# Kernel optimization log

Measured on AMD Instinct MI355X. Metric: run time of the kernel, lower is better.

The kernel has to match this reference:

```python
import jax, jax.numpy as jnp
import numpy as np
import math

B, S, D = 8, 2048, 512
H, DH = 8, 64  # heads, head dim

def setup_inputs() -> dict:
    key = jax.random.key(0)
    ks = jax.random.split(key, 13)
    w = 0.02
    return {
        "x_Q": jax.random.normal(ks[0], (B, S, D), jnp.float32),
        "x_K": jax.random.normal(ks[1], (B, S, D), jnp.float32),
        "x_V": jax.random.normal(ks[2], (B, S, D), jnp.float32),
        "Wq": jax.random.normal(ks[3], (H * DH, D), jnp.float32) * w,
        "bq": jnp.zeros((H * DH,), jnp.float32),
        "Wk": jax.random.normal(ks[4], (H * DH, D), jnp.float32) * w,
        "bk": jnp.zeros((H * DH,), jnp.float32),
        "Wv": jax.random.normal(ks[5], (H * DH, D), jnp.float32) * w,
        "bv": jnp.zeros((H * DH,), jnp.float32),
        "Wo": jax.random.normal(ks[6], (D, H * DH), jnp.float32) * w,
        "bo": jnp.zeros((D,), jnp.float32),
        "src_batch_lens": jax.random.randint(ks[7], (B,), 1, S + 1, jnp.int32),
    }

def reference(x_Q, x_K, x_V, Wq, bq, Wk, bk, Wv, bv, Wo, bo, src_batch_lens):
    b, s, _ = x_Q.shape
    # projections (torch Linear: x @ W.T + b), split into heads
    Q = (x_Q @ Wq.T + bq).reshape(b, s, H, DH)
    K = (x_K @ Wk.T + bk).reshape(b, s, H, DH)
    V = (x_V @ Wv.T + bv).reshape(b, s, H, DH)
    scale = 1.0 / math.sqrt(DH)
    # [b, h, q, k] scores
    scores = jnp.einsum('bqhd,bkhd->bhqk', Q * scale, K)
    # padding mask on key positions >= src_batch_lens[i], filled with -1e9
    key_mask = jnp.arange(s)[None, :] >= src_batch_lens[:, None]  # [b, k]
    scores = jnp.where(key_mask[:, None, None, :], -1.0e9, scores)
    attn = jax.nn.softmax(scores, axis=-1)  # dropout p=0.0 -> identity
    ctx = jnp.einsum('bhqk,bkhd->bqhd', attn, V).reshape(b, s, H * DH)
    return ctx @ Wo.T + bo
```

## Files before the change

### kernel.cpp

```cpp
#include <hip/hip_runtime.h>
#include <math.h>

#define NB 8
#define NS 2048
#define ND 512
#define NHH 8
#define NDH 64

typedef __attribute__((ext_vector_type(4))) float f32x4;
typedef __attribute__((ext_vector_type(8))) short bf16x8;
typedef unsigned short ush;

__device__ inline ush f2bf_rne(float f) {
    unsigned u = __float_as_uint(f);
    unsigned r = u + 0x7FFFu + ((u >> 16) & 1u);
    return (ush)(r >> 16);
}
__device__ inline float bf2f(ush h) { return __uint_as_float(((unsigned)h) << 16); }

__device__ inline unsigned cvt_pk_bf16(float lo, float hi) {
    unsigned r;
    asm("v_cvt_pk_bf16_f32 %0, %1, %2" : "=v"(r) : "v"(lo), "v"(hi));
    return r;
}

#if defined(__has_builtin)
#if __has_builtin(__builtin_amdgcn_exp2f)
#define EXP2F(x) __builtin_amdgcn_exp2f(x)
#else
#define EXP2F(x) exp2f(x)
#endif
#else
#define EXP2F(x) exp2f(x)
#endif

#define GLL16(gp, lp) __builtin_amdgcn_global_load_lds( \
    (const __attribute__((address_space(1))) unsigned int*)(gp), \
    (__attribute__((address_space(3))) unsigned int*)(lp), 16, 0, 0)

__global__ __launch_bounds__(256) void conv_w_kernel(
    const float* __restrict__ Wq, const float* __restrict__ Wk,
    const float* __restrict__ Wv, const float* __restrict__ Wo,
    ush* __restrict__ wbf, ush* __restrict__ wo_hi, ush* __restrict__ wo_lo)
{
    const int y = blockIdx.y;
    const int i = (blockIdx.x * 256 + threadIdx.x) * 4;
    if (y < 3) {
        const float* src = (y == 0) ? Wq : (y == 1) ? Wk : Wv;
        const float4 v = *(const float4*)&src[i];
        ushort4 o;
        o.x = f2bf_rne(v.x); o.y = f2bf_rne(v.y);
        o.z = f2bf_rne(v.z); o.w = f2bf_rne(v.w);
        *(ushort4*)&wbf[y * 262144 + i] = o;
    } else {
        const float4 v = *(const float4*)&Wo[i];
        ushort4 hi, lo;
        hi.x = f2bf_rne(v.x); lo.x = f2bf_rne(v.x - bf2f(hi.x));
        hi.y = f2bf_rne(v.y); lo.y = f2bf_rne(v.y - bf2f(hi.y));
        hi.z = f2bf_rne(v.z); lo.z = f2bf_rne(v.z - bf2f(hi.z));
        hi.w = f2bf_rne(v.w); lo.w = f2bf_rne(v.w - bf2f(hi.w));
        *(ushort4*)&wo_hi[i] = hi;
        *(ushort4*)&wo_lo[i] = lo;
    }
}

__global__ __launch_bounds__(256) void qkv_gemm_kernel(
    const float* __restrict__ xq, const float* __restrict__ xk, const float* __restrict__ xv,
    const ush* __restrict__ wbf,
    const float* __restrict__ bq, const float* __restrict__ bk, const float* __restrict__ bv,
    ush* __restrict__ Qb, ush* __restrict__ Kb, ush* __restrict__ VT)
{
    __shared__ ush As[4096];
    __shared__ ush Bs[4096];

    const int z = blockIdx.z;
    const float* X    = (z == 0) ? xq : (z == 1) ? xk : xv;
    const ush*   W    = wbf + z * 262144;
    const float* bias = (z == 0) ? bq : (z == 1) ? bk : bv;

    const int t = threadIdx.x;
    const int w = t >> 6, l = t & 63;
    const int l15 = l & 15, g = l >> 4;
    const int m0 = blockIdx.x * 128, n0 = blockIdx.y * 128;
    const int wm = (w & 1) << 6, wn = (w >> 1) << 6;

    const int srow = l >> 2;
    const int sg   = (l & 3) ^ ((srow + (srow >> 2)) & 3);
    const int fsw  = (g ^ ((l15 + (l15 >> 2)) & 3)) << 3;
    const int c0   = w * 2;

    f32x4 acc[4][4];
    #pragma unroll
    for (int i = 0; i < 4; ++i)
        #pragma unroll
        for (int j = 0; j < 4; ++j) acc[i][j] = (f32x4)(0.0f);

    for (int kt = 0; kt < 512; kt += 32) {
        const size_t ar0 = (size_t)(m0 + c0 * 16 + srow) * 512 + kt + sg * 8;
        const size_t ar1 = (size_t)(m0 + (c0 + 1) * 16 + srow) * 512 + kt + sg * 8;
        const float4 a0 = *(const float4*)&X[ar0];
        const float4 a1 = *(const float4*)&X[ar0 + 4];
        const float4 a2 = *(const float4*)&X[ar1];
        const float4 a3 = *(const float4*)&X[ar1 + 4];

        __syncthreads();

        GLL16(&W[(size_t)(n0 + c0 * 16 + srow) * 512 + kt + sg * 8], &Bs[c0 * 512 + l * 8]);
        GLL16(&W[(size_t)(n0 + (c0 + 1) * 16 + srow) * 512 + kt + sg * 8], &Bs[(c0 + 1) * 512 + l * 8]);

        uint4 u0, u1;
        u0.x = (unsigned)f2bf_rne(a0.x) | ((unsigned)f2bf_rne(a0.y) << 16);
        u0.y = (unsigned)f2bf_rne(a0.z) | ((unsigned)f2bf_rne(a0.w) << 16);
        u0.z = (unsigned)f2bf_rne(a1.x) | ((unsigned)f2bf_rne(a1.y) << 16);
        u0.w = (unsigned)f2bf_rne(a1.z) | ((unsigned)f2bf_rne(a1.w) << 16);
        u1.x = (unsigned)f2bf_rne(a2.x) | ((unsigned)f2bf_rne(a2.y) << 16);
        u1.y = (unsigned)f2bf_rne(a2.z) | ((unsigned)f2bf_rne(a2.w) << 16);
        u1.z = (unsigned)f2bf_rne(a3.x) | ((unsigned)f2bf_rne(a3.y) << 16);
        u1.w = (unsigned)f2bf_rne(a3.z) | ((unsigned)f2bf_rne(a3.w) << 16);
        *(uint4*)&As[c0 * 512 + l * 8] = u0;
        *(uint4*)&As[(c0 + 1) * 512 + l * 8] = u1;

        __syncthreads();

        bf16x8 af[4], bfr[4];
        #pragma unroll
        for (int mi = 0; mi < 4; ++mi)
            af[mi] = *(const bf16x8*)&As[(((w & 1) << 2) + mi) * 512 + l15 * 32 + fsw];
        #pragma unroll
        for (int ni = 0; ni < 4; ++ni)
            bfr[ni] = *(const bf16x8*)&Bs[(((w >> 1) << 2) + ni) * 512 + l15 * 32 + fsw];
        #pragma unroll
        for (int mi = 0; mi < 4; ++mi)
            #pragma unroll
            for (int ni = 0; ni < 4; ++ni)
                acc[mi][ni] = __builtin_amdgcn_mfma_f32_16x16x32_bf16(af[mi], bfr[ni], acc[mi][ni], 0, 0, 0);
    }

    const float qscale = (z == 0) ? 0.18033688011112042f : 1.0f;
    float bnv[4];
    #pragma unroll
    for (int ni = 0; ni < 4; ++ni) bnv[ni] = bias[n0 + wn + ni * 16 + l15];

    if (z < 2) {
        ush* O = (z == 0) ? Qb : Kb;
        #pragma unroll
        for (int mi = 0; mi < 4; ++mi) {
            #pragma unroll
            for (int ni = 0; ni < 4; ++ni) {
                const int n = n0 + wn + ni * 16 + l15;
                const int hh = n >> 6, dh = n & 63;
                #pragma unroll
                for (int r = 0; r < 4; ++r) {
                    const int m = m0 + wm + mi * 16 + (g << 2) + r;
                    const int bi = m >> 11, s = m & (NS - 1);
                    O[((size_t)(bi * 8 + hh) * 2048 + s) * 64 + dh] =
                        f2bf_rne((acc[mi][ni][r] + bnv[ni]) * qscale);
                }
            }
        }
    } else {
        #pragma unroll
        for (int mi = 0; mi < 4; ++mi) {
            #pragma unroll
            for (int ni = 0; ni < 4; ++ni) {
                const int n = n0 + wn + ni * 16 + l15;
                const int hh = n >> 6, dh = n & 63;
                const int mb = m0 + wm + mi * 16 + (g << 2);
                const int bi = mb >> 11, s = mb & (NS - 1);
                ushort4 pk;
                pk.x = f2bf_rne(acc[mi][ni][0] + bnv[ni]);
                pk.y = f2bf_rne(acc[mi][ni][1] + bnv[ni]);
                pk.z = f2bf_rne(acc[mi][ni][2] + bnv[ni]);
                pk.w = f2bf_rne(acc[mi][ni][3] + bnv[ni]);
                *(ushort4*)&VT[((size_t)(bi * 8 + hh) * 64 + dh) * 2048 + s] = pk;
            }
        }
    }
}

__global__ __launch_bounds__(256) void attn_kernel(
    ush* __restrict__ Qb, const ush* __restrict__ Kb,
    const ush* __restrict__ VT, const int* __restrict__ lens,
    ush* __restrict__ ctx_lo)
{
    __shared__ ush Ps[64 * 72];
    __shared__ ush Vt[4624];

    const int tid = threadIdx.x;
    const int w = tid >> 6, l = tid & 63;
    const int l15 = l & 15, g = l >> 4;

    const int id = blockIdx.x;
    const int h = id & 7, qt = (id >> 3) & 31, b = id >> 8;
    const int L = lens[b];
    const int q0 = qt << 6;
    const size_t bh = ((size_t)b * 8 + h) * 2048;

    const ush* qptr = Qb + (bh + q0 + w * 16 + l15) * 64 + g * 8;
    const bf16x8 qf0 = *(const bf16x8*)(qptr);
    const bf16x8 qf1 = *(const bf16x8*)(qptr + 32);

    const ush* kbase = Kb + (bh + l15) * 64 + g * 8;

    const int dv = tid >> 2, seg = (tid & 3) << 4;
    const ush* vbase = VT + ((size_t)(b * 8 + h) * 64 + dv) * 2048 + seg;
    ush* vt_w = &Vt[dv * 72 + ((dv >> 4) << 3) + seg];

    ush* psw = &Ps[(w * 16 + l15) * 72 + (g << 2)];
    const ush* pp = &Ps[(w * 16 + l15) * 72 + g * 8];

    bf16x8 ones;
    #pragma unroll
    for (int j = 0; j < 8; ++j) ones[j] = (short)0x3F80;

    f32x4 o[4];
    f32x4 ol = (f32x4)(0.0f);
    #pragma unroll
    for (int i = 0; i < 4; ++i) o[i] = (f32x4)(0.0f);

    auto tile = [&](int k0, bool masked) {
        const uint4 v0 = *(const uint4*)(vbase + k0);
        const uint4 v1 = *(const uint4*)(vbase + k0 + 8);

        f32x4 s[4];
        #pragma unroll
        for (int st = 0; st < 4; ++st) s[st] = (f32x4)(0.0f);
        const ush* kp = kbase + (size_t)k0 * 64;
        #pragma unroll
        for (int st = 0; st < 4; ++st) {
            const bf16x8 kf0 = *(const bf16x8*)(kp + st * 16 * 64);
            const bf16x8 kf1 = *(const bf16x8*)(kp + st * 16 * 64 + 32);
            s[st] = __builtin_amdgcn_mfma_f32_16x16x32_bf16(kf0, qf0, s[st], 0, 0, 0);
            s[st] = __builtin_amdgcn_mfma_f32_16x16x32_bf16(kf1, qf1, s[st], 0, 0, 0);
        }

        uint2 pk[4];
        #pragma unroll
        for (int st = 0; st < 4; ++st) {
            float p[4];
            #pragma unroll
            for (int r = 0; r < 4; ++r) {
                float e = EXP2F(s[st][r]);
                if (masked) {
                    const int key = k0 + st * 16 + (g << 2) + r;
                    e = (key < L) ? e : 0.0f;
                }
                p[r] = e;
            }
            pk[st].x = cvt_pk_bf16(p[0], p[1]);
            pk[st].y = cvt_pk_bf16(p[2], p[3]);
        }

        __syncthreads();
        *(uint4*)(vt_w) = v0;
        *(uint4*)(vt_w + 8) = v1;
        #pragma unroll
        for (int st = 0; st < 4; ++st)
            *(uint2*)(psw + st * 16) = pk[st];
        __syncthreads();

        const bf16x8 pf0 = *(const bf16x8*)(pp);
        const bf16x8 pf1 = *(const bf16x8*)(pp + 32);
        ol = __builtin_amdgcn_mfma_f32_16x16x32_bf16(pf0, ones, ol, 0, 0, 0);
        ol = __builtin_amdgcn_mfma_f32_16x16x32_bf16(pf1, ones, ol, 0, 0, 0);
        #pragma unroll
        for (int st2 = 0; st2 < 4; ++st2) {
            const ush* vp = &Vt[(st2 * 16 + l15) * 72 + (st2 << 3) + g * 8];
            const bf16x8 vf0 = *(const bf16x8*)(vp);
            const bf16x8 vf1 = *(const bf16x8*)(vp + 32);
            o[st2] = __builtin_amdgcn_mfma_f32_16x16x32_bf16(pf0, vf0, o[st2], 0, 0, 0);
            o[st2] = __builtin_amdgcn_mfma_f32_16x16x32_bf16(pf1, vf1, o[st2], 0, 0, 0);
        }
    };

    const int nfull = L >> 6;
    for (int kt = 0; kt < nfull; ++kt) tile(kt << 6, false);
    if (L & 63) tile(nfull << 6, true);

    #pragma unroll
    for (int r = 0; r < 4; ++r) {
        const float inv = 1.0f / ol[r];
        const size_t row = bh + q0 + w * 16 + (g << 2) + r;
        #pragma unroll
        for (int st2 = 0; st2 < 4; ++st2) {
            const float val = o[st2][r] * inv;
            const ush hi = f2bf_rne(val);
            const ush lo = f2bf_rne(val - bf2f(hi));
            Qb[row * 64 + st2 * 16 + l15] = hi;
            ctx_lo[row * 64 + st2 * 16 + l15] = lo;
        }
    }
}

__global__ __launch_bounds__(256) void out_gemm_kernel(
    const ush* __restrict__ ctx_hi, const ush* __restrict__ ctx_lo,
    const ush* __restrict__ wo_hi, const ush* __restrict__ wo_lo,
    const float* __restrict__ bo, float* __restrict__ out)
{
    __shared__ ush Ah[4096], Al[4096], Bh[4096], Bl[4096];

    const int t = threadIdx.x;
    const int w = t >> 6, l = t & 63;
    const int l15 = l & 15, g = l >> 4;
    const int m0 = blockIdx.x * 128, n0 = blockIdx.y * 128;
    const int wm = (w & 1) << 6, wn = (w >> 1) << 6;

    const int srow = l >> 2;
    const int sg   = (l & 3) ^ ((srow + (srow >> 2)) & 3);
    const int fsw  = (g ^ ((l15 + (l15 >> 2)) & 3)) << 3;
    const int c0   = w * 2;

    f32x4 acc[4][4];
    #pragma unroll
    for (int i = 0; i < 4; ++i)
        #pragma unroll
        for (int j = 0; j < 4; ++j) acc[i][j] = (f32x4)(0.0f);

    for (int kt = 0; kt < 512; kt += 32) {
        __syncthreads();
        #pragma unroll
        for (int cc = 0; cc < 2; ++cc) {
            const int c = c0 + cc;
            const int m = m0 + c * 16 + srow;
            const int k = kt + sg * 8;
            const size_t ga = ((size_t)((m >> 11) * 8 + (k >> 6)) * 2048 + (m & (NS - 1))) * 64 + (k & 63);
            GLL16(&ctx_hi[ga], &Ah[c * 512 + l * 8]);
            GLL16(&ctx_lo[ga], &Al[c * 512 + l * 8]);
            const size_t gb = (size_t)(n0 + c * 16 + srow) * 512 + kt + sg * 8;
            GLL16(&wo_hi[gb], &Bh[c * 512 + l * 8]);
            GLL16(&wo_lo[gb], &Bl[c * 512 + l * 8]);
        }
        __syncthreads();

        bf16x8 ah[4], al[4], bh4[4], bl4[4];
        #pragma unroll
        for (int mi = 0; mi < 4; ++mi) {
            const int off = (((w & 1) << 2) + mi) * 512 + l15 * 32 + fsw;
            ah[mi] = *(const bf16x8*)&Ah[off];
            al[mi] = *(const bf16x8*)&Al[off];
        }
        #pragma unroll
        for (int ni = 0; ni < 4; ++ni) {
            const int off = (((w >> 1) << 2) + ni) * 512 + l15 * 32 + fsw;
            bh4[ni] = *(const bf16x8*)&Bh[off];
            bl4[ni] = *(const bf16x8*)&Bl[off];
        }
        #pragma unroll
        for (int mi = 0; mi < 4; ++mi)
            #pragma unroll
            for (int ni = 0; ni < 4; ++ni) {
                acc[mi][ni] = __builtin_amdgcn_mfma_f32_16x16x32_bf16(ah[mi], bh4[ni], acc[mi][ni], 0, 0, 0);
                acc[mi][ni] = __builtin_amdgcn_mfma_f32_16x16x32_bf16(al[mi], bh4[ni], acc[mi][ni], 0, 0, 0);
                acc[mi][ni] = __builtin_amdgcn_mfma_f32_16x16x32_bf16(ah[mi], bl4[ni], acc[mi][ni], 0, 0, 0);
            }
    }

    float bov[4];
    #pragma unroll
    for (int ni = 0; ni < 4; ++ni) bov[ni] = bo[n0 + wn + ni * 16 + l15];

    #pragma unroll
    for (int mi = 0; mi < 4; ++mi)
        #pragma unroll
        for (int ni = 0; ni < 4; ++ni) {
            const int n = n0 + wn + ni * 16 + l15;
            #pragma unroll
            for (int r = 0; r < 4; ++r) {
                const int m = m0 + wm + mi * 16 + (g << 2) + r;
                out[(size_t)m * 512 + n] = acc[mi][ni][r] + bov[ni];
            }
        }
}

extern "C" void kernel_launch(void* const* d_in, const int* in_sizes, int n_in,
                              void* d_out, int out_size, void* d_ws, size_t ws_size,
                              hipStream_t stream)
{
    const float* xq   = (const float*)d_in[0];
    const float* xk   = (const float*)d_in[1];
    const float* xv   = (const float*)d_in[2];
    const float* Wq   = (const float*)d_in[3];
    const float* bq   = (const float*)d_in[4];
    const float* Wk   = (const float*)d_in[5];
    const float* bk   = (const float*)d_in[6];
    const float* Wv   = (const float*)d_in[7];
    const float* bv   = (const float*)d_in[8];
    const float* Wo   = (const float*)d_in[9];
    const float* bo   = (const float*)d_in[10];
    const int*   lens = (const int*)d_in[11];
    float* out = (float*)d_out;

    const size_t elems = (size_t)NB * NHH * NS * NDH;
    ush* Qb     = (ush*)d_ws;
    ush* Kb     = Qb + elems;
    ush* VT     = Kb + elems;
    ush* ctx_lo = VT + elems;
    ush* wbf    = ctx_lo + elems;
    ush* wo_hi  = wbf + 3 * 262144;
    ush* wo_lo  = wo_hi + 262144;

    const dim3 blk(256);
    conv_w_kernel<<<dim3(256, 4), blk, 0, stream>>>(Wq, Wk, Wv, Wo, wbf, wo_hi, wo_lo);
    qkv_gemm_kernel<<<dim3(128, 4, 3), blk, 0, stream>>>(
        xq, xk, xv, wbf, bq, bk, bv, Qb, Kb, VT);
    attn_kernel<<<dim3(NB * NHH * (NS / 64)), blk, 0, stream>>>(Qb, Kb, VT, lens, ctx_lo);
    out_gemm_kernel<<<dim3(128, 4), blk, 0, stream>>>(Qb, ctx_lo, wo_hi, wo_lo, bo, out);
}
```

Before: 357.0 us.

## Load V fragments directly from global into registers, drop LDS staging and barriers

The attention kernel no longer stages the transposed V tile through shared memory. Each wave now reads its V MFMA operands straight from global memory into registers, split into two halves issued around the QK MFMAs. This removes both __syncthreads per tile, since each wave only reads back the P rows it wrote itself. It also adds s_setprio around the MFMA blocks, at the cost of more global/L2 traffic (V is fetched redundantly by all 4 waves) and higher register pressure.

```diff
diff --git a/kernel.cpp b/kernel.cpp
--- a/kernel.cpp
+++ b/kernel.cpp
@@ -184,7 +184,6 @@
     ush* __restrict__ ctx_lo)
 {
     __shared__ ush Ps[64 * 72];
-    __shared__ ush Vt[4624];
 
     const int tid = threadIdx.x;
     const int w = tid >> 6, l = tid & 63;
@@ -201,10 +200,7 @@
     const bf16x8 qf1 = *(const bf16x8*)(qptr + 32);
 
     const ush* kbase = Kb + (bh + l15) * 64 + g * 8;
-
-    const int dv = tid >> 2, seg = (tid & 3) << 4;
-    const ush* vbase = VT + ((size_t)(b * 8 + h) * 64 + dv) * 2048 + seg;
-    ush* vt_w = &Vt[dv * 72 + ((dv >> 4) << 3) + seg];
+    const ush* vfbase = VT + bh * 64 + (size_t)l15 * 2048 + g * 8;
 
     ush* psw = &Ps[(w * 16 + l15) * 72 + (g << 2)];
     const ush* pp = &Ps[(w * 16 + l15) * 72 + g * 8];
@@ -219,13 +215,17 @@
     for (int i = 0; i < 4; ++i) o[i] = (f32x4)(0.0f);
 
     auto tile = [&](int k0, bool masked) {
-        const uint4 v0 = *(const uint4*)(vbase + k0);
-        const uint4 v1 = *(const uint4*)(vbase + k0 + 8);
+        const ush* vp = vfbase + k0;
+        bf16x8 vfA[4], vfB[4];
+        #pragma unroll
+        for (int st2 = 0; st2 < 4; ++st2)
+            vfA[st2] = *(const bf16x8*)(vp + st2 * 16 * 2048);
 
         f32x4 s[4];
         #pragma unroll
         for (int st = 0; st < 4; ++st) s[st] = (f32x4)(0.0f);
         const ush* kp = kbase + (size_t)k0 * 64;
+        __builtin_amdgcn_s_setprio(1);
         #pragma unroll
         for (int st = 0; st < 4; ++st) {
             const bf16x8 kf0 = *(const bf16x8*)(kp + st * 16 * 64);
@@ -233,6 +233,11 @@
             s[st] = __builtin_amdgcn_mfma_f32_16x16x32_bf16(kf0, qf0, s[st], 0, 0, 0);
             s[st] = __builtin_amdgcn_mfma_f32_16x16x32_bf16(kf1, qf1, s[st], 0, 0, 0);
         }
+        __builtin_amdgcn_s_setprio(0);
+
+        #pragma unroll
+        for (int st2 = 0; st2 < 4; ++st2)
+            vfB[st2] = *(const bf16x8*)(vp + st2 * 16 * 2048 + 32);
 
         uint2 pk[4];
         #pragma unroll
@@ -251,26 +256,22 @@
             pk[st].y = cvt_pk_bf16(p[2], p[3]);
         }
 
-        __syncthreads();
-        *(uint4*)(vt_w) = v0;
-        *(uint4*)(vt_w + 8) = v1;
         #pragma unroll
         for (int st = 0; st < 4; ++st)
             *(uint2*)(psw + st * 16) = pk[st];
-        __syncthreads();
-
         const bf16x8 pf0 = *(const bf16x8*)(pp);
         const bf16x8 pf1 = *(const bf16x8*)(pp + 32);
+
+        __builtin_amdgcn_s_setprio(1);
         ol = __builtin_amdgcn_mfma_f32_16x16x32_bf16(pf0, ones, ol, 0, 0, 0);
+        #pragma unroll
+        for (int st2 = 0; st2 < 4; ++st2)
+            o[st2] = __builtin_amdgcn_mfma_f32_16x16x32_bf16(pf0, vfA[st2], o[st2], 0, 0, 0);
         ol = __builtin_amdgcn_mfma_f32_16x16x32_bf16(pf1, ones, ol, 0, 0, 0);
         #pragma unroll
-        for (int st2 = 0; st2 < 4; ++st2) {
-            const ush* vp = &Vt[(st2 * 16 + l15) * 72 + (st2 << 3) + g * 8];
-            const bf16x8 vf0 = *(const bf16x8*)(vp);
-            const bf16x8 vf1 = *(const bf16x8*)(vp + 32);
-            o[st2] = __builtin_amdgcn_mfma_f32_16x16x32_bf16(pf0, vf0, o[st2], 0, 0, 0);
-            o[st2] = __builtin_amdgcn_mfma_f32_16x16x32_bf16(pf1, vf1, o[st2], 0, 0, 0);
-        }
+        for (int st2 = 0; st2 < 4; ++st2)
+            o[st2] = __builtin_amdgcn_mfma_f32_16x16x32_bf16(pf1, vfB[st2], o[st2], 0, 0, 0);
+        __builtin_amdgcn_s_setprio(0);
     };
 
     const int nfull = L >> 6;
```

Measured after the change: 443.1 us. 1.24x slower.

## Software-pipeline attention loop with double-buffered V tile and K prefetch

Applied to the files above, without the earlier changes.

Restructures the attention key loop so the next tile's K fragments and V data are loaded, and its QK^T MFMAs issued, while the current tile's softmax and PV MFMAs finish. V is double-buffered in LDS, which cuts the barriers per tile from two to one. It also wraps the MFMA bursts in s_setprio to favour matrix issue. This doubles the V LDS footprint and raises register pressure from the held K fragments, which may lower occupancy.

```diff
diff --git a/kernel.cpp b/kernel.cpp
--- a/kernel.cpp
+++ b/kernel.cpp
@@ -184,7 +184,7 @@
     ush* __restrict__ ctx_lo)
 {
     __shared__ ush Ps[64 * 72];
-    __shared__ ush Vt[4624];
+    __shared__ ush Vt[2 * 4624];
 
     const int tid = threadIdx.x;
     const int w = tid >> 6, l = tid & 63;
@@ -203,8 +203,8 @@
     const ush* kbase = Kb + (bh + l15) * 64 + g * 8;
 
     const int dv = tid >> 2, seg = (tid & 3) << 4;
-    const ush* vbase = VT + ((size_t)(b * 8 + h) * 64 + dv) * 2048 + seg;
-    ush* vt_w = &Vt[dv * 72 + ((dv >> 4) << 3) + seg];
+    const ush* vbase = VT + bh * 64 + (size_t)dv * 2048 + seg;
+    const int vt_off = dv * 72 + ((dv >> 4) << 3) + seg;
 
     ush* psw = &Ps[(w * 16 + l15) * 72 + (g << 2)];
     const ush* pp = &Ps[(w * 16 + l15) * 72 + g * 8];
@@ -218,31 +218,39 @@
     #pragma unroll
     for (int i = 0; i < 4; ++i) o[i] = (f32x4)(0.0f);
 
-    auto tile = [&](int k0, bool masked) {
-        const uint4 v0 = *(const uint4*)(vbase + k0);
-        const uint4 v1 = *(const uint4*)(vbase + k0 + 8);
-
-        f32x4 s[4];
-        #pragma unroll
-        for (int st = 0; st < 4; ++st) s[st] = (f32x4)(0.0f);
-        const ush* kp = kbase + (size_t)k0 * 64;
+    f32x4 sp[4];
+    const int T = (L + 63) >> 6;
+
+    {
+        const uint4 v0 = *(const uint4*)(vbase);
+        const uint4 v1 = *(const uint4*)(vbase + 8);
+        #pragma unroll
+        for (int st = 0; st < 4; ++st) sp[st] = (f32x4)(0.0f);
+        __builtin_amdgcn_s_setprio(1);
         #pragma unroll
         for (int st = 0; st < 4; ++st) {
-            const bf16x8 kf0 = *(const bf16x8*)(kp + st * 16 * 64);
-            const bf16x8 kf1 = *(const bf16x8*)(kp + st * 16 * 64 + 32);
-            s[st] = __builtin_amdgcn_mfma_f32_16x16x32_bf16(kf0, qf0, s[st], 0, 0, 0);
-            s[st] = __builtin_amdgcn_mfma_f32_16x16x32_bf16(kf1, qf1, s[st], 0, 0, 0);
-        }
-
+            const bf16x8 kf0 = *(const bf16x8*)(kbase + st * 1024);
+            const bf16x8 kf1 = *(const bf16x8*)(kbase + st * 1024 + 32);
+            sp[st] = __builtin_amdgcn_mfma_f32_16x16x32_bf16(kf0, qf0, sp[st], 0, 0, 0);
+            sp[st] = __builtin_amdgcn_mfma_f32_16x16x32_bf16(kf1, qf1, sp[st], 0, 0, 0);
+        }
+        __builtin_amdgcn_s_setprio(0);
+        ush* dst = &Vt[vt_off];
+        *(uint4*)dst = v0;
+        *(uint4*)(dst + 8) = v1;
+        __syncthreads();
+    }
+
+    auto finish = [&](const ush* vb, bool masked, int kb0) {
         uint2 pk[4];
         #pragma unroll
         for (int st = 0; st < 4; ++st) {
             float p[4];
             #pragma unroll
             for (int r = 0; r < 4; ++r) {
-                float e = EXP2F(s[st][r]);
+                float e = EXP2F(sp[st][r]);
                 if (masked) {
-                    const int key = k0 + st * 16 + (g << 2) + r;
+                    const int key = kb0 + st * 16 + (g << 2) + r;
                     e = (key < L) ? e : 0.0f;
                 }
                 p[r] = e;
@@ -250,32 +258,56 @@
             pk[st].x = cvt_pk_bf16(p[0], p[1]);
             pk[st].y = cvt_pk_bf16(p[2], p[3]);
         }
-
-        __syncthreads();
-        *(uint4*)(vt_w) = v0;
-        *(uint4*)(vt_w + 8) = v1;
         #pragma unroll
         for (int st = 0; st < 4; ++st)
             *(uint2*)(psw + st * 16) = pk[st];
-        __syncthreads();
-
         const bf16x8 pf0 = *(const bf16x8*)(pp);
         const bf16x8 pf1 = *(const bf16x8*)(pp + 32);
+        __builtin_amdgcn_s_setprio(1);
         ol = __builtin_amdgcn_mfma_f32_16x16x32_bf16(pf0, ones, ol, 0, 0, 0);
         ol = __builtin_amdgcn_mfma_f32_16x16x32_bf16(pf1, ones, ol, 0, 0, 0);
         #pragma unroll
         for (int st2 = 0; st2 < 4; ++st2) {
-            const ush* vp = &Vt[(st2 * 16 + l15) * 72 + (st2 << 3) + g * 8];
+            const ush* vp = vb + (st2 * 16 + l15) * 72 + (st2 << 3) + g * 8;
             const bf16x8 vf0 = *(const bf16x8*)(vp);
             const bf16x8 vf1 = *(const bf16x8*)(vp + 32);
             o[st2] = __builtin_amdgcn_mfma_f32_16x16x32_bf16(pf0, vf0, o[st2], 0, 0, 0);
             o[st2] = __builtin_amdgcn_mfma_f32_16x16x32_bf16(pf1, vf1, o[st2], 0, 0, 0);
         }
+        __builtin_amdgcn_s_setprio(0);
     };
 
-    const int nfull = L >> 6;
-    for (int kt = 0; kt < nfull; ++kt) tile(kt << 6, false);
-    if (L & 63) tile(nfull << 6, true);
+    for (int t = 1; t < T; ++t) {
+        const int k0 = t << 6;
+        const uint4 nv0 = *(const uint4*)(vbase + k0);
+        const uint4 nv1 = *(const uint4*)(vbase + k0 + 8);
+        bf16x8 kf[8];
+        const ush* kp = kbase + (size_t)k0 * 64;
+        #pragma unroll
+        for (int st = 0; st < 4; ++st) {
+            kf[2 * st]     = *(const bf16x8*)(kp + st * 1024);
+            kf[2 * st + 1] = *(const bf16x8*)(kp + st * 1024 + 32);
+        }
+
+        finish(&Vt[((t & 1) ^ 1) * 4624], false, 0);
+
+        #pragma unroll
+        for (int st = 0; st < 4; ++st) sp[st] = (f32x4)(0.0f);
+        __builtin_amdgcn_s_setprio(1);
+        #pragma unroll
+        for (int st = 0; st < 4; ++st) {
+            sp[st] = __builtin_amdgcn_mfma_f32_16x16x32_bf16(kf[2 * st], qf0, sp[st], 0, 0, 0);
+            sp[st] = __builtin_amdgcn_mfma_f32_16x16x32_bf16(kf[2 * st + 1], qf1, sp[st], 0, 0, 0);
+        }
+        __builtin_amdgcn_s_setprio(0);
+
+        ush* dst = &Vt[(t & 1) * 4624 + vt_off];
+        *(uint4*)dst = nv0;
+        *(uint4*)(dst + 8) = nv1;
+        __syncthreads();
+    }
+
+    finish(&Vt[((T - 1) & 1) * 4624], true, (T - 1) << 6);
 
     #pragma unroll
     for (int r = 0; r < 4; ++r) {
```

After: 354.8 us. About the same (-0.6%).
